# Kernel tuning notes

Measured on AMD Instinct MI355X. Metric: run time of the kernel, lower is better.

## Reference

```python
import jax, jax.numpy as jnp
import numpy as np

INF = jnp.float32(1e30)

# Jonker-Volgenant / Hungarian (shortest augmenting path) LSAP solver, faithful to
# scipy.optimize.linear_sum_assignment's algorithm, expressed with lax loops.

def _augment_row(C, carry, cur_row):
    u, v, col4row, row4col = carry
    n = C.shape[0]
    cur_row = jnp.asarray(cur_row, jnp.int32)

    def cond(st):
        return st[0] < 0

    def body(st):
        sink, i, minVal, remaining, SR, SC, spc, path = st
        SR = SR.at[i].set(True)
        # reduced costs from current row i to all still-remaining columns
        r = minVal + C[i] - u[i] - v
        upd = remaining & (r < spc)
        path = jnp.where(upd, i, path)
        spc = jnp.where(upd, r, spc)
        masked = jnp.where(remaining, spc, INF)
        j = jnp.argmin(masked).astype(jnp.int32)
        minVal = masked[j]
        unassigned = row4col[j] < 0
        sink = jnp.where(unassigned, j, jnp.int32(-1))
        i = jnp.where(unassigned, i, row4col[j])
        SC = SC.at[j].set(True)
        remaining = remaining.at[j].set(False)
        return (sink, i, minVal, remaining, SR, SC, spc, path)

    init = (jnp.int32(-1), cur_row, jnp.float32(0.0),
            jnp.ones(n, bool), jnp.zeros(n, bool), jnp.zeros(n, bool),
            jnp.full(n, INF), jnp.full(n, -1, jnp.int32))
    sink, _, minVal, _, SR, SC, spc, path = jax.lax.while_loop(cond, body, init)

    # dual variable updates (as in scipy's _lsap)
    u = u.at[cur_row].add(minVal)
    rows = jnp.arange(n)
    other = SR & (rows != cur_row)
    u = jnp.where(other, u + minVal - spc[col4row.clip(0)], u)
    v = jnp.where(SC, v - (minVal - spc), v)

    # augment along the alternating path back to cur_row
    def acond(st):
        return st[3]

    def abody(st):
        j, r4c, c4r, _ = st
        i = path[j]
        r4c = r4c.at[j].set(i)
        jn = c4r[i]
        c4r = c4r.at[i].set(j)
        return (jn, r4c, c4r, i != cur_row)

    _, row4col, col4row, _ = jax.lax.while_loop(
        acond, abody, (sink, row4col, col4row, jnp.bool_(True)))
    return (u, v, col4row, row4col)


def _lsap(C):
    # C: (n, n) float32 -> col4row (n,): optimal column assigned to each row
    n = C.shape[0]
    carry = (jnp.zeros(n, jnp.float32), jnp.zeros(n, jnp.float32),
             jnp.full(n, -1, jnp.int32), jnp.full(n, -1, jnp.int32))
    carry = jax.lax.fori_loop(0, n, lambda r, c: _augment_row(C, c, r), carry)
    return carry[2]


_solve = jax.jit(jax.vmap(_lsap))


def _normalize(D):
    # DETR-style per-sample cost normalization (monotone affine -> same optimum)
    d_min = D.min(axis=(1, 2), keepdims=True)
    d_rng = D.max(axis=(1, 2), keepdims=True) - d_min + 1e-8
    return (D - d_min) / d_rng


def setup_inputs() -> dict:
    key = jax.random.key(0)
    D = jax.random.normal(key, (128, 128, 128), dtype=jnp.float32)  # [B, N, N]
    return {"D": D}


def reference(D):
    col4row = _solve(_normalize(D))  # (B, n): row i -> column col4row[b, i]
    matched = jnp.take_along_axis(D, col4row[:, :, None], axis=2)[..., 0]  # (B, n)
    # torch: mean over matched entries per sample, then mean over batch; with
    # equal n per sample this equals a single global mean.
    return matched.mean()
```

## Files before the change

kernel.cpp:

```cpp
#include <hip/hip_runtime.h>

#define N 128
#define LSAP_INF 1e30f

__device__ __forceinline__ int rl_i(int v, int l) { return __builtin_amdgcn_readlane(v, l); }
__device__ __forceinline__ float rl_f(float v, int l) {
    return __int_as_float(__builtin_amdgcn_readlane(__float_as_int(v), l));
}
__device__ __forceinline__ int pick_i(int a0, int a1, int idx) {
    return (idx < 64) ? rl_i(a0, idx) : rl_i(a1, idx - 64);
}
__device__ __forceinline__ float pick_f(float a0, float a1, int idx) {
    return (idx < 64) ? rl_f(a0, idx) : rl_f(a1, idx - 64);
}
__device__ __forceinline__ float gather_f(float a0, float a1, int idx) {
    float x = __shfl(a0, idx & 63);
    float y = __shfl(a1, idx & 63);
    return (idx < 64) ? x : y;
}

__device__ __forceinline__ unsigned wave_min_key(unsigned x) {
#define DPP_STEP(ctrl)                                                                  \
    {                                                                                   \
        unsigned o = (unsigned)__builtin_amdgcn_update_dpp(                             \
            (int)0xFFFFFFFF, (int)x, (ctrl), 0xF, 0xF, false);                          \
        x = (o < x) ? o : x;                                                            \
    }
    DPP_STEP(0x111)
    DPP_STEP(0x112)
    DPP_STEP(0x114)
    DPP_STEP(0x118)
    DPP_STEP(0x142)
    DPP_STEP(0x143)
#undef DPP_STEP
    return (unsigned)rl_i((int)x, 63);
}

__device__ __forceinline__ void row_scan2(const float* Cs, const float* v_lds, int lane,
                                          float& m0, int& jm0, float& sm0,
                                          float& m1, int& jm1, float& sm1) {
    m0 = sm0 = m1 = sm1 = LSAP_INF;
    jm0 = jm1 = -1;
    for (int t = 0; t < N; ++t) {
        int j = (t + lane) & (N - 1);
        float vj = v_lds[j];
        float h0 = Cs[lane * N + j] - vj;
        float h1 = Cs[(lane + 64) * N + j] - vj;
        if (h0 < sm0) { if (h0 < m0) { sm0 = m0; m0 = h0; jm0 = j; } else sm0 = h0; }
        if (h1 < sm1) { if (h1 < m1) { sm1 = m1; m1 = h1; jm1 = j; } else sm1 = h1; }
    }
}

__global__ __launch_bounds__(64) void lsap_kernel(const float* __restrict__ D,
                                                  float* __restrict__ out,
                                                  float inv) {
    const int b = blockIdx.x;
    const int lane = threadIdx.x;
    const float* __restrict__ C = D + (size_t)b * N * N;

    __shared__ float Cs[N * N];
    __shared__ float v_lds[N];
    __shared__ float u_lds[N];
    __shared__ int rowsol_lds[N];
    __shared__ int colsol_lds[N];
    __shared__ int bid_lds[N];

    {
        const float4* __restrict__ src = (const float4*)C;
        float4* dst = (float4*)Cs;
#pragma unroll
        for (int t = 0; t < (N * N / 4) / 64; ++t) dst[t * 64 + lane] = src[t * 64 + lane];
    }
    __syncthreads();

    {
        float v0 = LSAP_INF, v1 = LSAP_INF;
        int am0 = -1, am1 = -1;
        for (int i = 0; i < N; ++i) {
            float c0 = Cs[i * N + lane];
            float c1 = Cs[i * N + lane + 64];
            if (c0 < v0) { v0 = c0; am0 = i; }
            if (c1 < v1) { v1 = c1; am1 = i; }
        }
        v_lds[lane] = v0;
        v_lds[lane + 64] = v1;
        rowsol_lds[lane] = -1; rowsol_lds[lane + 64] = -1;
        colsol_lds[lane] = -1; colsol_lds[lane + 64] = -1;
        __syncthreads();
        bid_lds[am0] = lane;
        bid_lds[am1] = lane + 64;
        __syncthreads();
        if (bid_lds[am0] == lane)      { colsol_lds[lane] = am0;      rowsol_lds[am0] = lane; }
        if (bid_lds[am1] == lane + 64) { colsol_lds[lane + 64] = am1; rowsol_lds[am1] = lane + 64; }
        __syncthreads();
    }

    {
        float m0, sm0, m1, sm1; int jm0, jm1;
        row_scan2(Cs, v_lds, lane, m0, jm0, sm0, m1, jm1, sm1);
        int j1_0 = rowsol_lds[lane];
        int j1_1 = rowsol_lds[lane + 64];
        __syncthreads();
        if (j1_0 >= 0) v_lds[j1_0] -= (sm0 - m0);
        if (j1_1 >= 0) v_lds[j1_1] -= (sm1 - m1);
        u_lds[lane]      = (j1_0 >= 0) ? sm0 : m0;
        u_lds[lane + 64] = (j1_1 >= 0) ? sm1 : m1;
        __syncthreads();
    }

    for (int round = 0; round < 16; ++round) {
        bool f0 = rowsol_lds[lane] < 0;
        bool f1 = rowsol_lds[lane + 64] < 0;
        if (__ballot(f0 || f1) == 0ULL) break;
        if ((round & 1) == 0) {
            float m0, sm0, m1, sm1; int jm0, jm1;
            row_scan2(Cs, v_lds, lane, m0, jm0, sm0, m1, jm1, sm1);
            bid_lds[lane] = -1;
            bid_lds[lane + 64] = -1;
            __syncthreads();
            if (f0) bid_lds[jm0] = lane;
            if (f1) bid_lds[jm1] = lane + 64;
            __syncthreads();
            if (f0 && bid_lds[jm0] == lane) {
                int old = colsol_lds[jm0];
                v_lds[jm0] -= (sm0 - m0);
                u_lds[lane] = sm0;
                colsol_lds[jm0] = lane;
                rowsol_lds[lane] = jm0;
                if (old >= 0) rowsol_lds[old] = -1;
            }
            if (f1 && bid_lds[jm1] == lane + 64) {
                int old = colsol_lds[jm1];
                v_lds[jm1] -= (sm1 - m1);
                u_lds[lane + 64] = sm1;
                colsol_lds[jm1] = lane + 64;
                rowsol_lds[lane + 64] = jm1;
                if (old >= 0) rowsol_lds[old] = -1;
            }
            __syncthreads();
        } else {
            bool g0 = colsol_lds[lane] < 0;
            bool g1 = colsol_lds[lane + 64] < 0;
            float m0 = LSAP_INF, sm0 = LSAP_INF, m1 = LSAP_INF, sm1 = LSAP_INF;
            int im0 = -1, im1 = -1;
            for (int t = 0; t < N; ++t) {
                int i = (t + lane) & (N - 1);
                float ui = u_lds[i];
                float y0 = Cs[i * N + lane] - ui;
                float y1 = Cs[i * N + lane + 64] - ui;
                if (y0 < sm0) { if (y0 < m0) { sm0 = m0; m0 = y0; im0 = i; } else sm0 = y0; }
                if (y1 < sm1) { if (y1 < m1) { sm1 = m1; m1 = y1; im1 = i; } else sm1 = y1; }
            }
            bid_lds[lane] = -1;
            bid_lds[lane + 64] = -1;
            __syncthreads();
            if (g0) bid_lds[im0] = lane;
            if (g1) bid_lds[im1] = lane + 64;
            __syncthreads();
            if (g0 && bid_lds[im0] == lane) {
                float un = u_lds[im0] - (sm0 - m0);
                u_lds[im0] = un;
                v_lds[lane] = Cs[im0 * N + lane] - un;
                int oldc = rowsol_lds[im0];
                rowsol_lds[im0] = lane;
                colsol_lds[lane] = im0;
                if (oldc >= 0) colsol_lds[oldc] = -1;
            }
            if (g1 && bid_lds[im1] == lane + 64) {
                float un = u_lds[im1] - (sm1 - m1);
                u_lds[im1] = un;
                v_lds[lane + 64] = Cs[im1 * N + lane + 64] - un;
                int oldc = rowsol_lds[im1];
                rowsol_lds[im1] = lane + 64;
                colsol_lds[lane + 64] = im1;
                if (oldc >= 0) colsol_lds[oldc] = -1;
            }
            __syncthreads();
        }
    }

    float umin0 = LSAP_INF, umin1 = LSAP_INF;
    for (int t = 0; t < N; ++t) {
        int j = (t + lane) & (N - 1);
        float vj = v_lds[j];
        umin0 = fminf(umin0, Cs[lane * N + j] - vj);
        umin1 = fminf(umin1, Cs[(lane + 64) * N + j] - vj);
    }

    float v0 = v_lds[lane], v1 = v_lds[lane + 64];
    int r4c0 = colsol_lds[lane], r4c1 = colsol_lds[lane + 64];
    int c4r0 = rowsol_lds[lane], c4r1 = rowsol_lds[lane + 64];
    float u0 = (c4r0 >= 0) ? u_lds[lane] : umin0;
    float u1 = (c4r1 >= 0) ? u_lds[lane + 64] : umin1;

    float urow0 = (r4c0 >= 0) ? gather_f(u0, u1, r4c0) : 0.f;
    float urow1 = (r4c1 >= 0) ? gather_f(u0, u1, r4c1) : 0.f;

    for (int cur = 0; cur < N; ++cur) {
        if (pick_i(c4r0, c4r1, cur) >= 0) continue;

        float spc0 = LSAP_INF, spc1 = LSAP_INF;
        int path0 = -1, path1 = -1;
        bool rem0 = true, rem1 = true;
        bool sc0 = false, sc1 = false;
        bool sr0 = false, sr1 = false;
        int i = cur;
        float u_i = pick_f(u0, u1, i);
        float minVal = 0.f;
        int sink;

        while (true) {
            if (lane == (i & 63)) { if (i < 64) sr0 = true; else sr1 = true; }
            float c0 = Cs[i * N + lane];
            float c1 = Cs[i * N + lane + 64];
            float base = minVal - u_i;
            float r0 = fmaxf(base + c0 - v0, 0.f);
            float r1 = fmaxf(base + c1 - v1, 0.f);
            if (rem0 && (r0 < spc0)) { spc0 = r0; path0 = i; }
            if (rem1 && (r1 < spc1)) { spc1 = r1; path1 = i; }
            float m0c = rem0 ? spc0 : LSAP_INF;
            float m1c = rem1 ? spc1 : LSAP_INF;
            unsigned k0 = (((unsigned)__float_as_int(m0c)) & ~127u) | (unsigned)lane;
            unsigned k1 = (((unsigned)__float_as_int(m1c)) & ~127u) | (unsigned)(lane + 64);
            unsigned kmin = wave_min_key((k0 < k1) ? k0 : k1);
            int j = (int)(kmin & 127u);
            minVal = __int_as_float((int)(kmin & ~127u));
            int rj = pick_i(r4c0, r4c1, j);
            float u_next = pick_f(urow0, urow1, j);
            if (lane == (j & 63)) {
                if (j < 64) { sc0 = true; rem0 = false; }
                else        { sc1 = true; rem1 = false; }
            }
            if (rj < 0) { sink = j; break; }
            i = rj;
            u_i = u_next;
        }

        {
            int g0i = (c4r0 < 0) ? 0 : c4r0;
            int g1i = (c4r1 < 0) ? 0 : c4r1;
            float g0 = gather_f(spc0, spc1, g0i);
            float g1 = gather_f(spc0, spc1, g1i);

            if (cur == lane)          u0 += minVal;
            else if (sr0)             u0 += minVal - g0;
            if (cur == lane + 64)     u1 += minVal;
            else if (sr1)             u1 += minVal - g1;
            if (sc0) v0 -= minVal - spc0;
            if (sc1) v1 -= minVal - spc1;
        }

        int j = sink;
        while (true) {
            int ip = pick_i(path0, path1, j);
            if (lane == (j & 63)) { if (j < 64) r4c0 = ip; else r4c1 = ip; }
            int jn = pick_i(c4r0, c4r1, ip);
            if (lane == (ip & 63)) { if (ip < 64) c4r0 = j; else c4r1 = j; }
            if (ip == cur) break;
            j = jn;
        }

        urow0 = (r4c0 >= 0) ? gather_f(u0, u1, r4c0) : 0.f;
        urow1 = (r4c1 >= 0) ? gather_f(u0, u1, r4c1) : 0.f;
    }

    float s = Cs[lane * N + c4r0] + Cs[(lane + 64) * N + c4r1];
#pragma unroll
    for (int off = 32; off >= 1; off >>= 1) s += __shfl_xor(s, off);
    if (lane == 0) atomicAdd(out, s * inv);
}

extern "C" void kernel_launch(void* const* d_in, const int* in_sizes, int n_in,
                              void* d_out, int out_size, void* d_ws, size_t ws_size,
                              hipStream_t stream) {
    const float* D = (const float*)d_in[0];
    float* out = (float*)d_out;
    const int B = in_sizes[0] / (N * N);
    hipMemsetAsync(out, 0, sizeof(float), stream);
    lsap_kernel<<<B, 64, 0, stream>>>(D, out, 1.0f / (float)(B * N));
}
```

Measured before the change: 289.2 us.

## Speculatively prefetch cost rows for the next two likely columns in the Dijkstra loop

Inside the shortest-augmenting-path loop, the kernel now also finds the second and third smallest remaining keys and loads the C rows of their matched rows from LDS ahead of time. If the next chosen column matches one of these guesses, the prefetched row is used and the dependent LDS load is skipped. This aims to hide LDS latency on the serial critical path. The cost is two extra wave-wide min reductions and four extra LDS loads per iteration, and guesses may often miss because spc changes each step.

```diff
diff --git a/kernel.cpp b/kernel.cpp
--- a/kernel.cpp
+++ b/kernel.cpp
@@ -208,32 +208,51 @@
         float u_i = pick_f(u0, u1, i);
         float minVal = 0.f;
         int sink;
+        int spec_ja = -2, spec_jb = -2;
+        float sa0 = 0.f, sa1 = 0.f, sb0 = 0.f, sb1 = 0.f;
+        float c0 = Cs[i * N + lane];
+        float c1 = Cs[i * N + lane + 64];
 
         while (true) {
             if (lane == (i & 63)) { if (i < 64) sr0 = true; else sr1 = true; }
-            float c0 = Cs[i * N + lane];
-            float c1 = Cs[i * N + lane + 64];
             float base = minVal - u_i;
             float r0 = fmaxf(base + c0 - v0, 0.f);
             float r1 = fmaxf(base + c1 - v1, 0.f);
             if (rem0 && (r0 < spc0)) { spc0 = r0; path0 = i; }
             if (rem1 && (r1 < spc1)) { spc1 = r1; path1 = i; }
-            float m0c = rem0 ? spc0 : LSAP_INF;
-            float m1c = rem1 ? spc1 : LSAP_INF;
-            unsigned k0 = (((unsigned)__float_as_int(m0c)) & ~127u) | (unsigned)lane;
-            unsigned k1 = (((unsigned)__float_as_int(m1c)) & ~127u) | (unsigned)(lane + 64);
+            unsigned k0 = rem0 ? ((((unsigned)__float_as_int(spc0)) & ~127u) | (unsigned)lane)
+                               : 0xFFFFFFFFu;
+            unsigned k1 = rem1 ? ((((unsigned)__float_as_int(spc1)) & ~127u) | (unsigned)(lane + 64))
+                               : 0xFFFFFFFFu;
             unsigned kmin = wave_min_key((k0 < k1) ? k0 : k1);
             int j = (int)(kmin & 127u);
             minVal = __int_as_float((int)(kmin & ~127u));
             int rj = pick_i(r4c0, r4c1, j);
-            float u_next = pick_f(urow0, urow1, j);
+            float u_nx = pick_f(urow0, urow1, j);
             if (lane == (j & 63)) {
                 if (j < 64) { sc0 = true; rem0 = false; }
                 else        { sc1 = true; rem1 = false; }
             }
             if (rj < 0) { sink = j; break; }
-            i = rj;
-            u_i = u_next;
+            bool hit_a = (j == spec_ja), hit_b = (j == spec_jb);
+            if (hit_a)      { c0 = sa0; c1 = sa1; }
+            else if (hit_b) { c0 = sb0; c1 = sb1; }
+            else            { c0 = Cs[rj * N + lane]; c1 = Cs[rj * N + lane + 64]; }
+            if (lane == (j & 63)) { if (j < 64) k0 = 0xFFFFFFFFu; else k1 = 0xFFFFFFFFu; }
+            unsigned kmin2 = wave_min_key((k0 < k1) ? k0 : k1);
+            int j2 = (int)(kmin2 & 127u);
+            spec_ja = (kmin2 == 0xFFFFFFFFu) ? -2 : j2;
+            int rj2 = pick_i(r4c0, r4c1, j2);
+            int ra = (rj2 < 0) ? 0 : rj2;
+            sa0 = Cs[ra * N + lane]; sa1 = Cs[ra * N + lane + 64];
+            if (lane == (j2 & 63)) { if (j2 < 64) k0 = 0xFFFFFFFFu; else k1 = 0xFFFFFFFFu; }
+            unsigned kmin3 = wave_min_key((k0 < k1) ? k0 : k1);
+            int j3 = (int)(kmin3 & 127u);
+            spec_jb = (kmin3 == 0xFFFFFFFFu) ? -2 : j3;
+            int rj3 = pick_i(r4c0, r4c1, j3);
+            int rb = (rj3 < 0) ? 0 : rj3;
+            sb0 = Cs[rb * N + lane]; sb1 = Cs[rb * N + lane + 64];
+            i = rj; u_i = u_nx;
         }
 
         {
```

New measurement: 347.6 us. 20.2% more time.

## Add Jonker-Volgenant augmenting row reduction phase before shortest-path augmentation

Applied to the files above, without the earlier changes.

Inserts an augmenting row reduction loop, as in the LAPJV heuristic, between column reduction and the shortest augmenting path phase. Each pass takes a free row, finds its best and second-best reduced costs with DPP wave reductions, assigns the row to its best column, and evicts that column's previous owner. The phase is capped by an iteration limit and a stagnation counter. The aim is to cut the number of rows left free, so fewer costly Dijkstra-style augmentations remain. The cost is extra serial iterations, and tie handling may alter the final assignment if costs are degenerate.

```diff
diff --git a/kernel.cpp b/kernel.cpp
--- a/kernel.cpp
+++ b/kernel.cpp
@@ -34,6 +34,21 @@
     DPP_STEP(0x143)
 #undef DPP_STEP
     return (unsigned)rl_i((int)x, 63);
+}
+
+__device__ __forceinline__ float wave_min_f32(float x) {
+    const int infb = __float_as_int(LSAP_INF);
+#define DPP_STEP(ctrl)                                                                   \
+    x = fminf(x, __int_as_float(__builtin_amdgcn_update_dpp(                             \
+               infb, __float_as_int(x), (ctrl), 0xF, 0xF, false)));
+    DPP_STEP(0x111)
+    DPP_STEP(0x112)
+    DPP_STEP(0x114)
+    DPP_STEP(0x118)
+    DPP_STEP(0x142)
+    DPP_STEP(0x143)
+#undef DPP_STEP
+    return rl_f(x, 63);
 }
 
 __device__ __forceinline__ void row_scan2(const float* Cs, const float* v_lds, int lane,
@@ -179,6 +194,51 @@
         }
     }
 
+    float v0 = v_lds[lane], v1 = v_lds[lane + 64];
+    float u0 = u_lds[lane], u1 = u_lds[lane + 64];
+    int r4c0 = colsol_lds[lane], r4c1 = colsol_lds[lane + 64];
+    int c4r0 = rowsol_lds[lane], c4r1 = rowsol_lds[lane + 64];
+
+    {
+        int cap = 224, stagnant = 0, prev_nfree = N + 1;
+        while (cap-- > 0) {
+            unsigned long long ba = __ballot(c4r0 < 0);
+            unsigned long long bb = __ballot(c4r1 < 0);
+            if (!(ba | bb)) break;
+            int nfree = __popcll(ba) + __popcll(bb);
+            if (nfree < prev_nfree) { prev_nfree = nfree; stagnant = 0; }
+            else if (++stagnant >= 48) break;
+            int i = ba ? __builtin_ctzll(ba) : (64 + __builtin_ctzll(bb));
+            float c0 = Cs[i * N + lane];
+            float c1 = Cs[i * N + lane + 64];
+            float h0 = c0 - v0;
+            float h1 = c1 - v1;
+            float m = wave_min_f32(fminf(h0, h1));
+            unsigned long long e0 = __ballot(h0 == m);
+            int jm;
+            if (e0) jm = __builtin_ctzll(e0);
+            else    jm = 64 + __builtin_ctzll(__ballot(h1 == m));
+            float h0m = (lane == jm) ? LSAP_INF : h0;
+            float h1m = (lane + 64 == jm) ? LSAP_INF : h1;
+            float sm = wave_min_f32(fminf(h0m, h1m));
+            int old = pick_i(r4c0, r4c1, jm);
+            if (lane == (i & 63)) {
+                if (i < 64) { c4r0 = jm; u0 = sm; }
+                else        { c4r1 = jm; u1 = sm; }
+            }
+            if (lane == (jm & 63)) {
+                if (jm < 64) { v0 = c0 - sm; r4c0 = i; }
+                else         { v1 = c1 - sm; r4c1 = i; }
+            }
+            if (old >= 0 && lane == (old & 63)) {
+                if (old < 64) c4r0 = -1; else c4r1 = -1;
+            }
+        }
+    }
+
+    v_lds[lane] = v0;
+    v_lds[lane + 64] = v1;
+    __syncthreads();
     float umin0 = LSAP_INF, umin1 = LSAP_INF;
     for (int t = 0; t < N; ++t) {
         int j = (t + lane) & (N - 1);
@@ -186,12 +246,8 @@
         umin0 = fminf(umin0, Cs[lane * N + j] - vj);
         umin1 = fminf(umin1, Cs[(lane + 64) * N + j] - vj);
     }
-
-    float v0 = v_lds[lane], v1 = v_lds[lane + 64];
-    int r4c0 = colsol_lds[lane], r4c1 = colsol_lds[lane + 64];
-    int c4r0 = rowsol_lds[lane], c4r1 = rowsol_lds[lane + 64];
-    float u0 = (c4r0 >= 0) ? u_lds[lane] : umin0;
-    float u1 = (c4r1 >= 0) ? u_lds[lane + 64] : umin1;
+    if (c4r0 < 0) u0 = umin0;
+    if (c4r1 < 0) u1 = umin1;
 
     float urow0 = (r4c0 >= 0) ? gather_f(u0, u1, r4c0) : 0.f;
     float urow1 = (r4c1 >= 0) ? gather_f(u0, u1, r4c1) : 0.f;
```

Result: slower. 319.8 us (+10.6%).

## Track second-smallest key in wave reduction and prefetch its cost row speculatively

Applied to the files above, without the earlier changes.

The wave-wide argmin now computes the two smallest keys in a single DPP pass. The second-best column's row index, dual value and cost-row values are fetched ahead of time, so if the next iteration picks that column the serial dependency on an LDS load and readlane is skipped. This is aimed at the latency-bound Dijkstra inner loop. In exchange every step does roughly twice the DPP work, issues extra LDS loads that often go unused, and needs more registers. The speculation may rarely hit, because a column is removed once it is picked.

```diff
diff --git a/kernel.cpp b/kernel.cpp
--- a/kernel.cpp
+++ b/kernel.cpp
@@ -19,21 +19,25 @@
     return (idx < 64) ? x : y;
 }
 
-__device__ __forceinline__ unsigned wave_min_key(unsigned x) {
-#define DPP_STEP(ctrl)                                                                  \
+__device__ __forceinline__ void wave_min2_key(unsigned a, unsigned b,
+                                              unsigned& m, unsigned& m2) {
+    unsigned x = (a < b) ? a : b;
+    unsigned y = (a < b) ? b : a;
+#define DPP2(ctrl)                                                                      \
     {                                                                                   \
-        unsigned o = (unsigned)__builtin_amdgcn_update_dpp(                             \
+        unsigned ox = (unsigned)__builtin_amdgcn_update_dpp(                            \
             (int)0xFFFFFFFF, (int)x, (ctrl), 0xF, 0xF, false);                          \
-        x = (o < x) ? o : x;                                                            \
-    }
-    DPP_STEP(0x111)
-    DPP_STEP(0x112)
-    DPP_STEP(0x114)
-    DPP_STEP(0x118)
-    DPP_STEP(0x142)
-    DPP_STEP(0x143)
-#undef DPP_STEP
-    return (unsigned)rl_i((int)x, 63);
+        unsigned oy = (unsigned)__builtin_amdgcn_update_dpp(                            \
+            (int)0xFFFFFFFF, (int)y, (ctrl), 0xF, 0xF, false);                          \
+        unsigned mx = (x < ox) ? ox : x;                                                \
+        x = (x < ox) ? x : ox;                                                          \
+        y = (y < oy) ? y : oy;                                                          \
+        y = (y < mx) ? y : mx;                                                          \
+    }
+    DPP2(0x111) DPP2(0x112) DPP2(0x114) DPP2(0x118) DPP2(0x142) DPP2(0x143)
+#undef DPP2
+    m  = (unsigned)rl_i((int)x, 63);
+    m2 = (unsigned)rl_i((int)y, 63);
 }
 
 __device__ __forceinline__ void row_scan2(const float* Cs, const float* v_lds, int lane,
@@ -208,11 +212,13 @@
         float u_i = pick_f(u0, u1, i);
         float minVal = 0.f;
         int sink;
+        float c0 = Cs[i * N + lane];
+        float c1 = Cs[i * N + lane + 64];
+        int pj2 = -3, pi2 = 0;
+        float pu2 = 0.f, pc0 = 0.f, pc1 = 0.f;
 
         while (true) {
             if (lane == (i & 63)) { if (i < 64) sr0 = true; else sr1 = true; }
-            float c0 = Cs[i * N + lane];
-            float c1 = Cs[i * N + lane + 64];
             float base = minVal - u_i;
             float r0 = fmaxf(base + c0 - v0, 0.f);
             float r1 = fmaxf(base + c1 - v1, 0.f);
@@ -222,18 +228,35 @@
             float m1c = rem1 ? spc1 : LSAP_INF;
             unsigned k0 = (((unsigned)__float_as_int(m0c)) & ~127u) | (unsigned)lane;
             unsigned k1 = (((unsigned)__float_as_int(m1c)) & ~127u) | (unsigned)(lane + 64);
-            unsigned kmin = wave_min_key((k0 < k1) ? k0 : k1);
+            unsigned kmin, kmin2;
+            wave_min2_key(k0, k1, kmin, kmin2);
             int j = (int)(kmin & 127u);
             minVal = __int_as_float((int)(kmin & ~127u));
-            int rj = pick_i(r4c0, r4c1, j);
-            float u_next = pick_f(urow0, urow1, j);
+            bool hit = (j == pj2);
+            int rj    = hit ? pi2 : pick_i(r4c0, r4c1, j);
+            float u_nx = hit ? pu2 : pick_f(urow0, urow1, j);
             if (lane == (j & 63)) {
                 if (j < 64) { sc0 = true; rem0 = false; }
                 else        { sc1 = true; rem1 = false; }
             }
             if (rj < 0) { sink = j; break; }
-            i = rj;
-            u_i = u_next;
+            float nc0, nc1;
+            if (hit) { nc0 = pc0; nc1 = pc1; }
+            else     { nc0 = Cs[rj * N + lane]; nc1 = Cs[rj * N + lane + 64]; }
+            int j2 = (int)(kmin2 & 127u);
+            if (kmin2 != 0xFFFFFFFFu) {
+                pj2 = j2;
+                int rj2 = pick_i(r4c0, r4c1, j2);
+                pi2 = rj2;
+                pu2 = pick_f(urow0, urow1, j2);
+                int ra = (rj2 < 0) ? 0 : rj2;
+                pc0 = Cs[ra * N + lane];
+                pc1 = Cs[ra * N + lane + 64];
+            } else {
+                pj2 = -3;
+            }
+            c0 = nc0; c1 = nc1;
+            i = rj; u_i = u_nx;
         }
 
         {
```

New measurement: 335.7 us. 1.16x slower.
